# Kernel optimization log

Measured on AMD Instinct MI355X. Metric: run time of the kernel, lower is better.

Reference implementation:

```python
import jax, jax.numpy as jnp
import numpy as np

N_NODES = 100000
N_EDGES = 6400000
F_IN, F_HID, F_OUT = 5, 5, 10


def setup_inputs() -> dict:
    key = jax.random.key(0)
    ks = jax.random.split(key, 9)
    x = jax.random.normal(ks[0], (N_NODES, F_IN), dtype=jnp.float32)
    src = jax.random.randint(ks[1], (N_EDGES,), 0, N_NODES, dtype=jnp.int32)
    dst = jax.random.randint(ks[2], (N_EDGES,), 0, N_NODES, dtype=jnp.int32)
    s1 = 1.0 / np.sqrt(F_IN)
    s2 = 1.0 / np.sqrt(F_HID)
    W_self1 = jax.random.uniform(ks[3], (F_IN, F_HID), jnp.float32, -s1, s1)
    W_neigh1 = jax.random.uniform(ks[4], (F_IN, F_HID), jnp.float32, -s1, s1)
    b1 = jnp.zeros((F_HID,), jnp.float32)
    W_self2 = jax.random.uniform(ks[5], (F_HID, F_OUT), jnp.float32, -s2, s2)
    W_neigh2 = jax.random.uniform(ks[6], (F_HID, F_OUT), jnp.float32, -s2, s2)
    b2 = jnp.zeros((F_OUT,), jnp.float32)
    return {"x": x, "src": src, "dst": dst,
            "W_self1": W_self1, "W_neigh1": W_neigh1, "b1": b1,
            "W_self2": W_self2, "W_neigh2": W_neigh2, "b2": b2}


def _sage_mean(h, src, dst, W_self, W_neigh, b):
    # DGL SAGEConv (mean): out = h @ W_self + mean_{u->v}(h_u) @ W_neigh + b
    msg = h[src]                                        # [E, F] gather
    agg = jax.ops.segment_sum(msg, dst, num_segments=N_NODES)   # [N, F]
    deg = jax.ops.segment_sum(jnp.ones((src.shape[0],), h.dtype), dst,
                              num_segments=N_NODES)     # [N]
    h_neigh = agg / jnp.maximum(deg, 1.0)[:, None]
    return h @ W_self + h_neigh @ W_neigh + b


def reference(x, src, dst, W_self1, W_neigh1, b1, W_self2, W_neigh2, b2):
    h = jax.nn.sigmoid(_sage_mean(x, src, dst, W_self1, W_neigh1, b1))
    out = jax.nn.sigmoid(_sage_mean(h, src, dst, W_self2, W_neigh2, b2))
    return out
```

## Files before the change

### kernel.cpp

```cpp
#include <hip/hip_runtime.h>
#include <hip/hip_fp16.h>
#include <math.h>


#define F_IN  5
#define F_HID 5
#define F_OUT 10

#define NBSHIFT 7
#define NPB     (1 << NBSHIFT)
#define PBLK    1024
#define CHUNK   8192
#define EPT     8
#define BSTRIDE 9216
#define SBLK    512
#define SPT     18
#define LPN2    8
#define LBLK    256

__global__ void init_cursors(int* __restrict__ bcursor, int NB) {
    int t = blockIdx.x * blockDim.x + threadIdx.x;
    if (t < NB) bcursor[t] = t * BSTRIDE;
}

__global__ void partition(const int* __restrict__ src, const int* __restrict__ dst,
                          int* __restrict__ bcursor, int* __restrict__ packed,
                          int E, int NB) {
    __shared__ int cnt[PBLK], s[PBLK], excl[PBLK], adj[PBLK];
    __shared__ int buf[CHUNK];
    __shared__ unsigned char dlow[CHUNK];
    int t = threadIdx.x;
    cnt[t] = 0;
    __syncthreads();
    int base = blockIdx.x * CHUNK;
    int end  = min(base + CHUNK, E);
    int esd[EPT];
    int ebp[EPT];
    #pragma unroll
    for (int j = 0; j < EPT; ++j) {
        int i = base + t + j * PBLK;
        if (i < end) {
            int sv = src[i], d = dst[i];
            int b  = d >> NBSHIFT;
            int p  = atomicAdd(&cnt[b], 1);
            esd[j] = sv | ((d & (NPB - 1)) << 17);
            ebp[j] = (b << 14) | p;
        }
    }
    __syncthreads();
    s[t] = cnt[t];
    __syncthreads();
    for (int off = 1; off < PBLK; off <<= 1) {
        int v = (t >= off) ? s[t - off] : 0;
        __syncthreads();
        s[t] += v;
        __syncthreads();
    }
    excl[t] = s[t] - cnt[t];
    __syncthreads();
    if (t < NB) {
        int cb = cnt[t];
        int go = cb ? atomicAdd(&bcursor[t], cb) : 0;
        adj[t] = go - excl[t];
    }
    __syncthreads();
    #pragma unroll
    for (int j = 0; j < EPT; ++j) {
        int i = base + t + j * PBLK;
        if (i < end) {
            int b   = ebp[j] >> 14;
            int pos = excl[b] + (ebp[j] & 0x3FFF);
            buf[pos]  = (esd[j] & 0x1FFFF) | (b << 17);
            dlow[pos] = (unsigned char)(esd[j] >> 17);
        }
    }
    __syncthreads();
    int cval = end - base;
    for (int p = t; p < cval; p += PBLK) {
        int e = buf[p];
        int b = e >> 17;
        packed[adj[b] + p] = (e & 0x1FFFF) | ((int)dlow[p] << 17);
    }
}

__device__ __forceinline__ float sigmoidf(float v) {
    return 1.0f / (1.0f + __expf(-v));
}

__global__ void __launch_bounds__(SBLK, 8)
sortagg1(const float* __restrict__ x, int* __restrict__ packed,
         const int* __restrict__ bcursor,
         const float* __restrict__ Ws, const float* __restrict__ Wn,
         const float* __restrict__ bias,
         uint4* __restrict__ hp, int* __restrict__ starts,
         int* __restrict__ degs, int N) {
    __shared__ int buf[BSTRIDE];
    __shared__ int ncnt[NPB], nst[NPB];
    int b = blockIdx.x, t = threadIdx.x;
    int s0  = b * BSTRIDE;
    int cnt = min(bcursor[b] - s0, BSTRIDE);
    if (t < NPB) ncnt[t] = 0;
    __syncthreads();
    int myv[SPT];
    short myp[SPT];
    #pragma unroll
    for (int j = 0; j < SPT; ++j) {
        int i = t + j * SBLK;
        if (i < cnt) {
            int e = packed[s0 + i];
            myv[j] = e;
            myp[j] = (short)atomicAdd(&ncnt[(e >> 17) & (NPB - 1)], 1);
        }
    }
    __syncthreads();
    int v = (t < NPB) ? ncnt[t] : 0;
    int run = v;
    __syncthreads();
    if (t < NPB) nst[t] = run;
    __syncthreads();
    for (int off = 1; off < NPB; off <<= 1) {
        int u = (t < NPB && t >= off) ? nst[t - off] : 0;
        __syncthreads();
        if (t < NPB) nst[t] += u;
        __syncthreads();
    }
    if (t < NPB) {
        nst[t] -= v;
        int node = (b << NBSHIFT) + t;
        if (node < N) { starts[node] = s0 + nst[t]; degs[node] = v; }
    }
    __syncthreads();
    #pragma unroll
    for (int j = 0; j < SPT; ++j) {
        int i = t + j * SBLK;
        if (i < cnt) {
            int e  = myv[j];
            buf[nst[(e >> 17) & (NPB - 1)] + (int)myp[j]] = e;
        }
    }
    __syncthreads();
    for (int i = t; i < cnt; i += SBLK)
        packed[s0 + i] = buf[i] & 0x1FFFF;
    int sub = t & 3, ln = t >> 2;
    int node = (b << NBSHIFT) + ln;
    float a0 = 0, a1 = 0, a2 = 0, a3 = 0, a4 = 0;
    int dg = 0;
    if (node < N) {
        int st = nst[ln];
        dg = ncnt[ln];
        for (int k = sub; k < dg; k += 4) {
            int u = buf[st + k] & 0x1FFFF;
            const float* fr = x + (size_t)u * 5;
            float4 a = *(const float4*)fr;
            float  e4 = fr[4];
            a0 += a.x; a1 += a.y; a2 += a.z; a3 += a.w; a4 += e4;
        }
    }
    #pragma unroll
    for (int off = 2; off > 0; off >>= 1) {
        a0 += __shfl_down(a0, off, 4);
        a1 += __shfl_down(a1, off, 4);
        a2 += __shfl_down(a2, off, 4);
        a3 += __shfl_down(a3, off, 4);
        a4 += __shfl_down(a4, off, 4);
    }
    if (sub != 0 || node >= N) return;
    float rd = 1.0f / fmaxf((float)dg, 1.0f);
    float ni[F_IN] = { a0 * rd, a1 * rd, a2 * rd, a3 * rd, a4 * rd };
    float xi[F_IN];
    const float* xr = x + (size_t)node * 5;
    #pragma unroll
    for (int f = 0; f < F_IN; ++f) xi[f] = xr[f];
    unsigned short hu[8];
    #pragma unroll
    for (int j = 0; j < F_HID; ++j) {
        float acc = bias[j];
        #pragma unroll
        for (int f = 0; f < F_IN; ++f)
            acc += xi[f] * Ws[f * F_HID + j] + ni[f] * Wn[f * F_HID + j];
        hu[j] = __half_as_ushort(__float2half_rn(sigmoidf(acc)));
    }
    hu[5] = hu[6] = hu[7] = 0;
    uint4 o;
    o.x = (unsigned)hu[0] | ((unsigned)hu[1] << 16);
    o.y = (unsigned)hu[2] | ((unsigned)hu[3] << 16);
    o.z = (unsigned)hu[4] | ((unsigned)hu[5] << 16);
    o.w = 0;
    hp[node] = o;
}

__global__ void layer2(const uint4* __restrict__ hp, const int* __restrict__ eidx,
                       const int* __restrict__ starts, const int* __restrict__ degs,
                       const float* __restrict__ Ws, const float* __restrict__ Wn,
                       const float* __restrict__ b,
                       float* __restrict__ out, int N) {
    int tid = blockIdx.x * blockDim.x + threadIdx.x;
    int v   = tid >> 3;
    int sub = threadIdx.x & (LPN2 - 1);
    if (v >= N) return;
    int st = starts[v], dg = degs[v];
    float s0 = 0, s1 = 0, s2 = 0, s3 = 0, s4 = 0;
    for (int k = sub; k < dg; k += LPN2) {
        int u = eidx[st + k];
        uint4 q = hp[u];
        float2 f01 = __half22float2(*(const __half2*)&q.x);
        float2 f23 = __half22float2(*(const __half2*)&q.y);
        float2 f45 = __half22float2(*(const __half2*)&q.z);
        s0 += f01.x; s1 += f01.y; s2 += f23.x; s3 += f23.y; s4 += f45.x;
    }
    #pragma unroll
    for (int off = LPN2 / 2; off > 0; off >>= 1) {
        s0 += __shfl_down(s0, off, LPN2);
        s1 += __shfl_down(s1, off, LPN2);
        s2 += __shfl_down(s2, off, LPN2);
        s3 += __shfl_down(s3, off, LPN2);
        s4 += __shfl_down(s4, off, LPN2);
    }
    if (sub != 0) return;
    float rd = 1.0f / fmaxf((float)dg, 1.0f);
    float ni[F_HID] = { s0 * rd, s1 * rd, s2 * rd, s3 * rd, s4 * rd };
    uint4 q = hp[v];
    float2 f01 = __half22float2(*(const __half2*)&q.x);
    float2 f23 = __half22float2(*(const __half2*)&q.y);
    float2 f45 = __half22float2(*(const __half2*)&q.z);
    float hi[F_HID] = { f01.x, f01.y, f23.x, f23.y, f45.x };
    #pragma unroll
    for (int j = 0; j < F_OUT; ++j) {
        float acc = b[j];
        #pragma unroll
        for (int f = 0; f < F_HID; ++f)
            acc += hi[f] * Ws[f * F_OUT + j] + ni[f] * Wn[f * F_OUT + j];
        out[(size_t)v * F_OUT + j] = sigmoidf(acc);
    }
}

extern "C" void kernel_launch(void* const* d_in, const int* in_sizes, int n_in,
                              void* d_out, int out_size, void* d_ws, size_t ws_size,
                              hipStream_t stream) {
    const float* x   = (const float*)d_in[0];
    const int*   src = (const int*)d_in[1];
    const int*   dst = (const int*)d_in[2];
    const float* Ws1 = (const float*)d_in[3];
    const float* Wn1 = (const float*)d_in[4];
    const float* b1  = (const float*)d_in[5];
    const float* Ws2 = (const float*)d_in[6];
    const float* Wn2 = (const float*)d_in[7];
    const float* b2  = (const float*)d_in[8];
    float* out = (float*)d_out;

    const int N  = in_sizes[0] / F_IN;
    const int E  = in_sizes[1];
    const int NB = (N + NPB - 1) >> NBSHIFT;

    int*   bcursor = (int*)d_ws;
    int*   starts  = bcursor + 1024;
    int*   degs    = starts + N;
    int*   packed  = degs + N;
    uint4* hp      = (uint4*)(packed + (size_t)NB * BSTRIDE);

    const int ablocks = (E + CHUNK - 1) / CHUNK;
    const int lgrid   = ((size_t)N * LPN2 + LBLK - 1) / LBLK;

    init_cursors<<<1, 1024, 0, stream>>>(bcursor, NB);
    partition<<<ablocks, PBLK, 0, stream>>>(src, dst, bcursor, packed, E, NB);
    sortagg1<<<NB, SBLK, 0, stream>>>(x, packed, bcursor, Ws1, Wn1, b1,
                                      hp, starts, degs, N);
    layer2<<<lgrid, LBLK, 0, stream>>>(hp, packed, starts, degs, Ws2, Wn2, b2, out, N);
}
```

Baseline: 218.6 us.

## Pack layer-1 inputs to fp16 16-byte rows and use wave-shuffle scans

A new prep kernel converts x into a 16-byte-aligned fp16 row per node and also initialises the bucket cursors. The layer-1 neighbour gather then does one aligned uint4 load per edge instead of an unaligned float4 plus a scalar load. The block-wide prefix scans in partition and sortagg1 are replaced by wavefront shuffle scans, which cuts the number of barriers. The cost is one extra pass over x and fp16 rounding of the input features.

```diff
diff --git a/kernel.cpp b/kernel.cpp
--- a/kernel.cpp
+++ b/kernel.cpp
@@ -18,18 +18,40 @@
 #define LPN2    8
 #define LBLK    256
 
-__global__ void init_cursors(int* __restrict__ bcursor, int NB) {
-    int t = blockIdx.x * blockDim.x + threadIdx.x;
-    if (t < NB) bcursor[t] = t * BSTRIDE;
+__device__ __forceinline__ float sigmoidf(float v) {
+    return 1.0f / (1.0f + __expf(-v));
+}
+
+__global__ void prep(const float* __restrict__ x, uint4* __restrict__ xh,
+                     int* __restrict__ bcursor, int N, int NB) {
+    int v = blockIdx.x * blockDim.x + threadIdx.x;
+    if (v < NB) bcursor[v] = v * BSTRIDE;
+    if (v >= N) return;
+    const float* xr = x + (size_t)v * 5;
+    float4 a = *(const float4*)xr;
+    float a4 = xr[4];
+    unsigned short h0 = __half_as_ushort(__float2half_rn(a.x));
+    unsigned short h1 = __half_as_ushort(__float2half_rn(a.y));
+    unsigned short h2 = __half_as_ushort(__float2half_rn(a.z));
+    unsigned short h3 = __half_as_ushort(__float2half_rn(a.w));
+    unsigned short h4 = __half_as_ushort(__float2half_rn(a4));
+    uint4 o;
+    o.x = (unsigned)h0 | ((unsigned)h1 << 16);
+    o.y = (unsigned)h2 | ((unsigned)h3 << 16);
+    o.z = (unsigned)h4;
+    o.w = 0;
+    xh[v] = o;
 }
 
 __global__ void partition(const int* __restrict__ src, const int* __restrict__ dst,
                           int* __restrict__ bcursor, int* __restrict__ packed,
                           int E, int NB) {
-    __shared__ int cnt[PBLK], s[PBLK], excl[PBLK], adj[PBLK];
+    __shared__ int cnt[PBLK], excl[PBLK], adj[PBLK];
+    __shared__ int wsum[16];
     __shared__ int buf[CHUNK];
     __shared__ unsigned char dlow[CHUNK];
     int t = threadIdx.x;
+    int lane = t & 63, w = t >> 6;
     cnt[t] = 0;
     __syncthreads();
     int base = blockIdx.x * CHUNK;
@@ -48,15 +70,27 @@
         }
     }
     __syncthreads();
-    s[t] = cnt[t];
-    __syncthreads();
-    for (int off = 1; off < PBLK; off <<= 1) {
-        int v = (t >= off) ? s[t - off] : 0;
-        __syncthreads();
-        s[t] += v;
-        __syncthreads();
-    }
-    excl[t] = s[t] - cnt[t];
+    int v = cnt[t];
+    int incl = v;
+    #pragma unroll
+    for (int off = 1; off < 64; off <<= 1) {
+        int u = __shfl_up(incl, off, 64);
+        if (lane >= off) incl += u;
+    }
+    if (lane == 63) wsum[w] = incl;
+    __syncthreads();
+    if (t < 16) {
+        int s = wsum[t];
+        #pragma unroll
+        for (int off = 1; off < 16; off <<= 1) {
+            int u = __shfl_up(s, off, 16);
+            if (t >= off) s += u;
+        }
+        wsum[t] = s;
+    }
+    __syncthreads();
+    int wbase = (w > 0) ? wsum[w - 1] : 0;
+    excl[t] = incl - v + wbase;
     __syncthreads();
     if (t < NB) {
         int cb = cnt[t];
@@ -83,12 +117,8 @@
     }
 }
 
-__device__ __forceinline__ float sigmoidf(float v) {
-    return 1.0f / (1.0f + __expf(-v));
-}
-
 __global__ void __launch_bounds__(SBLK, 8)
-sortagg1(const float* __restrict__ x, int* __restrict__ packed,
+sortagg1(const uint4* __restrict__ xh, int* __restrict__ packed,
          const int* __restrict__ bcursor,
          const float* __restrict__ Ws, const float* __restrict__ Wn,
          const float* __restrict__ bias,
@@ -96,6 +126,7 @@
          int* __restrict__ degs, int N) {
     __shared__ int buf[BSTRIDE];
     __shared__ int ncnt[NPB], nst[NPB];
+    __shared__ int w0sum;
     int b = blockIdx.x, t = threadIdx.x;
     int s0  = b * BSTRIDE;
     int cnt = min(bcursor[b] - s0, BSTRIDE);
@@ -113,28 +144,31 @@
         }
     }
     __syncthreads();
-    int v = (t < NPB) ? ncnt[t] : 0;
-    int run = v;
-    __syncthreads();
-    if (t < NPB) nst[t] = run;
-    __syncthreads();
-    for (int off = 1; off < NPB; off <<= 1) {
-        int u = (t < NPB && t >= off) ? nst[t - off] : 0;
-        __syncthreads();
-        if (t < NPB) nst[t] += u;
-        __syncthreads();
-    }
     if (t < NPB) {
-        nst[t] -= v;
+        int lane = t & 63;
+        int v = ncnt[t];
+        int incl = v;
+        #pragma unroll
+        for (int off = 1; off < 64; off <<= 1) {
+            int u = __shfl_up(incl, off, 64);
+            if (lane >= off) incl += u;
+        }
+        if (t == 63) w0sum = incl;
+        nst[t] = incl - v;
+    }
+    __syncthreads();
+    if (t >= 64 && t < NPB) nst[t] += w0sum;
+    __syncthreads();
+    if (t < NPB) {
         int node = (b << NBSHIFT) + t;
-        if (node < N) { starts[node] = s0 + nst[t]; degs[node] = v; }
+        if (node < N) { starts[node] = s0 + nst[t]; degs[node] = ncnt[t]; }
     }
     __syncthreads();
     #pragma unroll
     for (int j = 0; j < SPT; ++j) {
         int i = t + j * SBLK;
         if (i < cnt) {
-            int e  = myv[j];
+            int e = myv[j];
             buf[nst[(e >> 17) & (NPB - 1)] + (int)myp[j]] = e;
         }
     }
@@ -150,10 +184,11 @@
         dg = ncnt[ln];
         for (int k = sub; k < dg; k += 4) {
             int u = buf[st + k] & 0x1FFFF;
-            const float* fr = x + (size_t)u * 5;
-            float4 a = *(const float4*)fr;
-            float  e4 = fr[4];
-            a0 += a.x; a1 += a.y; a2 += a.z; a3 += a.w; a4 += e4;
+            uint4 q = xh[u];
+            float2 f01 = __half22float2(*(const __half2*)&q.x);
+            float2 f23 = __half22float2(*(const __half2*)&q.y);
+            float2 f45 = __half22float2(*(const __half2*)&q.z);
+            a0 += f01.x; a1 += f01.y; a2 += f23.x; a3 += f23.y; a4 += f45.x;
         }
     }
     #pragma unroll
@@ -167,11 +202,12 @@
     if (sub != 0 || node >= N) return;
     float rd = 1.0f / fmaxf((float)dg, 1.0f);
     float ni[F_IN] = { a0 * rd, a1 * rd, a2 * rd, a3 * rd, a4 * rd };
-    float xi[F_IN];
-    const float* xr = x + (size_t)node * 5;
-    #pragma unroll
-    for (int f = 0; f < F_IN; ++f) xi[f] = xr[f];
-    unsigned short hu[8];
+    uint4 qs = xh[node];
+    float2 s01 = __half22float2(*(const __half2*)&qs.x);
+    float2 s23 = __half22float2(*(const __half2*)&qs.y);
+    float2 s45 = __half22float2(*(const __half2*)&qs.z);
+    float xi[F_IN] = { s01.x, s01.y, s23.x, s23.y, s45.x };
+    unsigned short hu[6];
     #pragma unroll
     for (int j = 0; j < F_HID; ++j) {
         float acc = bias[j];
@@ -180,11 +216,11 @@
             acc += xi[f] * Ws[f * F_HID + j] + ni[f] * Wn[f * F_HID + j];
         hu[j] = __half_as_ushort(__float2half_rn(sigmoidf(acc)));
     }
-    hu[5] = hu[6] = hu[7] = 0;
+    hu[5] = 0;
     uint4 o;
     o.x = (unsigned)hu[0] | ((unsigned)hu[1] << 16);
     o.y = (unsigned)hu[2] | ((unsigned)hu[3] << 16);
-    o.z = (unsigned)hu[4] | ((unsigned)hu[5] << 16);
+    o.z = (unsigned)hu[4];
     o.w = 0;
     hp[node] = o;
 }
@@ -253,17 +289,19 @@
     const int NB = (N + NPB - 1) >> NBSHIFT;
 
     int*   bcursor = (int*)d_ws;
-    int*   starts  = bcursor + 1024;
+    uint4* xh      = (uint4*)(bcursor + 1024);
+    int*   starts  = (int*)(xh + N);
     int*   degs    = starts + N;
     int*   packed  = degs + N;
     uint4* hp      = (uint4*)(packed + (size_t)NB * BSTRIDE);
 
     const int ablocks = (E + CHUNK - 1) / CHUNK;
+    const int pgrid   = (N + 255) / 256;
     const int lgrid   = ((size_t)N * LPN2 + LBLK - 1) / LBLK;
 
-    init_cursors<<<1, 1024, 0, stream>>>(bcursor, NB);
+    prep<<<pgrid, 256, 0, stream>>>(x, xh, bcursor, N, NB);
     partition<<<ablocks, PBLK, 0, stream>>>(src, dst, bcursor, packed, E, NB);
-    sortagg1<<<NB, SBLK, 0, stream>>>(x, packed, bcursor, Ws1, Wn1, b1,
+    sortagg1<<<NB, SBLK, 0, stream>>>(xh, packed, bcursor, Ws1, Wn1, b1,
                                       hp, starts, degs, N);
     layer2<<<lgrid, LBLK, 0, stream>>>(hp, packed, starts, degs, Ws2, Wn2, b2, out, N);
 }
```

Result: faster. 209.7 us (-4.1%).
